# Kernel optimization log

Hardware: AMD Instinct MI355X
Metric: run time of the kernel (lower is better)

The kernel has to match this reference:

```python
import jax, jax.numpy as jnp
import numpy as np

B, T, D = 64, 2048, 512


def setup_inputs() -> dict:
    key = jax.random.key(0)
    ks = jax.random.split(key, 6)
    lim_tau = 1.0 / np.sqrt(2 * D)  # torch Linear default init bound
    lim_mem = 1.0 / np.sqrt(D)
    return {
        "x": jax.random.normal(ks[0], (B, T, D), dtype=jnp.float32),
        "tau_w": jax.random.uniform(ks[1], (D, 2 * D), jnp.float32, -lim_tau, lim_tau),
        "tau_b": jax.random.uniform(ks[2], (D,), jnp.float32, -lim_tau, lim_tau),
        "mem_w": jax.random.uniform(ks[3], (D, D), jnp.float32, -lim_mem, lim_mem),
        "mem_b": jax.random.uniform(ks[4], (D,), jnp.float32, -lim_mem, lim_mem),
        "log_thresh": jnp.zeros((D,), jnp.float32),
    }


def reference(x, tau_w, tau_b, mem_w, mem_b, log_thresh):
    b, t, d = x.shape
    thr = jax.nn.sigmoid(log_thresh)  # [D]

    def step(carry, xt):
        v, tau = carry  # each [B, D]
        # liquid time-constant gate: sigmoid(Linear([xt, tau]))
        tau = jax.nn.sigmoid(jnp.concatenate([xt, tau], axis=-1) @ tau_w.T + tau_b)
        alpha = jnp.exp(-1.0 / (tau + 1e-6))
        v = alpha * v + (1.0 - alpha) * (xt @ mem_w.T + mem_b)
        s = (v >= thr).astype(x.dtype)  # spike
        v = v * (1.0 - s)  # hard reset
        return (v, tau), s

    x_tbd = jnp.swapaxes(x, 0, 1)  # [T, B, D] for scan
    init = (jnp.zeros((b, d), x.dtype), jnp.ones((b, d), x.dtype))
    (v, tau), spikes = jax.lax.scan(step, init, x_tbd)
    return jnp.swapaxes(spikes, 0, 1), tau, v  # [B,T,D], [B,D], [B,D]
```

## Files before the change

kernel.cpp:

```cpp
#include <hip/hip_runtime.h>
#include <math.h>

#define B_ 64
#define T_ 2048
#define D_ 512
#define BT_ (B_ * T_)
#define XWORDS (B_ * D_)

typedef unsigned long long u64;

__global__ void prep_weights(const float* __restrict__ tau_w,
                             const float* __restrict__ mem_w,
                             float* __restrict__ Wcat,
                             float* __restrict__ WTh) {
    int idx = blockIdx.x * 256 + threadIdx.x;
    {
        int k = idx >> 10, j = idx & 1023;
        float v = (j < 512) ? tau_w[j * 1024 + k] : mem_w[(j - 512) * 512 + k];
        Wcat[idx] = v;
    }
    if (idx < 512 * 512) {
        int k = idx >> 9, d = idx & 511;
        WTh[idx] = tau_w[d * 1024 + 512 + k];
    }
}

__global__ __launch_bounds__(256, 2)
void gemm_xw(const float* __restrict__ X, const float* __restrict__ Wc,
             const float* __restrict__ tau_b, const float* __restrict__ mem_b,
             float* __restrict__ Aout, float* __restrict__ Mout) {
    __shared__ __align__(16) float As[16][128];
    __shared__ __align__(16) float Bs[16][128];
    const int bn = blockIdx.x;
    const int bm = blockIdx.y;
    const int tid = threadIdx.x;
    const int tm = (tid >> 4) << 3;
    const int tn = (tid & 15) << 3;
    const int m0 = bm * 128, n0 = bn * 128;

    const float4* X4 = (const float4*)X;
    const float4* Wc4 = (const float4*)Wc;

    float acc[8][8];
#pragma unroll
    for (int i = 0; i < 8; i++)
#pragma unroll
        for (int j = 0; j < 8; j++) acc[i][j] = 0.0f;

    const int ar = tid >> 1;
    const int ac2 = (tid & 1) * 2;
    const int bkr = tid >> 4;
    const int bc = (tid & 15) * 2;

    for (int kt = 0; kt < 512; kt += 16) {
        float4 av0 = X4[(m0 + ar) * 128 + (kt >> 2) + ac2];
        float4 av1 = X4[(m0 + ar) * 128 + (kt >> 2) + ac2 + 1];
        float4 bv0 = Wc4[(kt + bkr) * 256 + bn * 32 + bc];
        float4 bv1 = Wc4[(kt + bkr) * 256 + bn * 32 + bc + 1];
        __syncthreads();
        As[ac2 * 4 + 0][ar] = av0.x;
        As[ac2 * 4 + 1][ar] = av0.y;
        As[ac2 * 4 + 2][ar] = av0.z;
        As[ac2 * 4 + 3][ar] = av0.w;
        As[ac2 * 4 + 4][ar] = av1.x;
        As[ac2 * 4 + 5][ar] = av1.y;
        As[ac2 * 4 + 6][ar] = av1.z;
        As[ac2 * 4 + 7][ar] = av1.w;
        *(float4*)&Bs[bkr][bc * 4] = bv0;
        *(float4*)&Bs[bkr][bc * 4 + 4] = bv1;
        __syncthreads();
#pragma unroll
        for (int kk = 0; kk < 16; kk++) {
            float4 a0 = *(const float4*)&As[kk][tm];
            float4 a1 = *(const float4*)&As[kk][tm + 4];
            float4 b0 = *(const float4*)&Bs[kk][tn];
            float4 b1 = *(const float4*)&Bs[kk][tn + 4];
            float av[8] = {a0.x, a0.y, a0.z, a0.w, a1.x, a1.y, a1.z, a1.w};
            float bv[8] = {b0.x, b0.y, b0.z, b0.w, b1.x, b1.y, b1.z, b1.w};
#pragma unroll
            for (int i = 0; i < 8; i++)
#pragma unroll
                for (int j = 0; j < 8; j++)
                    acc[i][j] = fmaf(av[i], bv[j], acc[i][j]);
        }
    }

    const bool isA = (bn < 4);
    float* Cout = isA ? Aout : Mout;
    const float* bias = isA ? tau_b : mem_b;
    const int ncol0 = (isA ? n0 : n0 - 512) + tn;
    float bj[8];
#pragma unroll
    for (int j = 0; j < 8; j++) bj[j] = bias[ncol0 + j];
#pragma unroll
    for (int i = 0; i < 8; i++) {
        size_t off = (size_t)(m0 + tm + i) * 512 + ncol0;
        float4 o0, o1;
        o0.x = acc[i][0] + bj[0]; o0.y = acc[i][1] + bj[1];
        o0.z = acc[i][2] + bj[2]; o0.w = acc[i][3] + bj[3];
        o1.x = acc[i][4] + bj[4]; o1.y = acc[i][5] + bj[5];
        o1.z = acc[i][6] + bj[6]; o1.w = acc[i][7] + bj[7];
        *(float4*)&Cout[off] = o0;
        *(float4*)&Cout[off + 4] = o1;
    }
}

__global__ void init_sync(u64* __restrict__ xchg, int* __restrict__ ctr) {
    int idx = blockIdx.x * 256 + threadIdx.x;
    if (idx < 2 * XWORDS) xchg[idx] = (idx < XWORDS) ? 0x3F800000ull : 0ull;
    if (idx < 16) ctr[idx] = 0;
}

__global__ __launch_bounds__(512)
__attribute__((amdgpu_waves_per_eu(2, 2)))
void scan_lds(const float* __restrict__ WTh,
              const float* __restrict__ Mm,
              const float* __restrict__ log_thresh,
              float* __restrict__ AmOut,
              float* __restrict__ OutTail,
              u64* __restrict__ xchg,
              int* __restrict__ ctr) {
    __shared__ __align__(16) float4 w_lds[8192];
    __shared__ __align__(16) float tau_s[2][512];
    __shared__ __align__(16) float part[2][16][64];
    __shared__ int role_s;

    const int tid = threadIdx.x;

    if (tid == 0) {
        unsigned xcd;
        asm volatile("s_getreg_b32 %0, hwreg(HW_REG_XCC_ID)" : "=s"(xcd));
        xcd &= 7;
        int rank = atomicAdd(&ctr[xcd], 1) & 31;
        role_s = ((rank & 7) << 8) | ((int)xcd * 4 + (rank >> 3));
    }
    __syncthreads();
    const int sg = role_s >> 8;
    const int bp = role_s & 255;

    {
        const int ch = tid & 63;
        const int kr8 = tid >> 6;
        float* wl = (float*)w_lds;
        for (int i = 0; i < 64; i++) {
            int krow = i * 8 + kr8;
            float val = WTh[krow * 512 + sg * 64 + ch];
            wl[(krow >> 2) * 256 + ch * 4 + (krow & 3)] = val;
        }
    }

    const int eb = tid >> 6;
    const int ech = tid & 63;
    const int gch = sg * 64 + ech;
    float thr = 0.f, v = 0.f, tau_keep = 0.f;
    if (tid < 128) thr = 1.0f / (1.0f + expf(-log_thresh[gch]));
    size_t abase = ((size_t)(bp * 2 + eb) * T_) * D_ + gch;

    const int cp = tid & 31;
    const int ks = tid >> 5;

    const int gb = (tid >> 7) & 1;
    const int ge = tid & 127;

    __syncthreads();

    for (int c = 1; c <= T_; c++) {
        float a_in = 0.f, m_in = 0.f;
        if (tid < 128) { a_in = AmOut[abase]; m_in = Mm[abase]; }

        if (tid < 256) {
            const u64* src = xchg + (size_t)((c - 1) & 1) * XWORDS
                                  + (bp * 2 + gb) * 512 + ge * 4;
            const unsigned tgt = (unsigned)(c - 1);
            u64 v0, v1, v2, v3;
            int guard = 0;
            do {
                v0 = __hip_atomic_load(src + 0, __ATOMIC_RELAXED,
                                       __HIP_MEMORY_SCOPE_AGENT);
                v1 = __hip_atomic_load(src + 1, __ATOMIC_RELAXED,
                                       __HIP_MEMORY_SCOPE_AGENT);
                v2 = __hip_atomic_load(src + 2, __ATOMIC_RELAXED,
                                       __HIP_MEMORY_SCOPE_AGENT);
                v3 = __hip_atomic_load(src + 3, __ATOMIC_RELAXED,
                                       __HIP_MEMORY_SCOPE_AGENT);
            } while ((((unsigned)(v0 >> 32) < tgt) |
                      ((unsigned)(v1 >> 32) < tgt) |
                      ((unsigned)(v2 >> 32) < tgt) |
                      ((unsigned)(v3 >> 32) < tgt)) && ++guard < (1 << 22));
            float4 tv = make_float4(__uint_as_float((unsigned)v0),
                                    __uint_as_float((unsigned)v1),
                                    __uint_as_float((unsigned)v2),
                                    __uint_as_float((unsigned)v3));
            *(float4*)&tau_s[gb][ge * 4] = tv;
        }
        __syncthreads();

        float acc00 = 0.f, acc01 = 0.f, acc10 = 0.f, acc11 = 0.f;
#pragma unroll
        for (int q = 0; q < 8; q++) {
            const int qq = ks * 8 + q;
            float4 wA = w_lds[qq * 64 + cp];
            float4 wB = w_lds[qq * 64 + cp + 32];
            float4 t0 = *(const float4*)&tau_s[0][qq * 4];
            float4 t1 = *(const float4*)&tau_s[1][qq * 4];
            acc00 = fmaf(t0.x, wA.x, acc00); acc00 = fmaf(t0.y, wA.y, acc00);
            acc00 = fmaf(t0.z, wA.z, acc00); acc00 = fmaf(t0.w, wA.w, acc00);
            acc01 = fmaf(t0.x, wB.x, acc01); acc01 = fmaf(t0.y, wB.y, acc01);
            acc01 = fmaf(t0.z, wB.z, acc01); acc01 = fmaf(t0.w, wB.w, acc01);
            acc10 = fmaf(t1.x, wA.x, acc10); acc10 = fmaf(t1.y, wA.y, acc10);
            acc10 = fmaf(t1.z, wA.z, acc10); acc10 = fmaf(t1.w, wA.w, acc10);
            acc11 = fmaf(t1.x, wB.x, acc11); acc11 = fmaf(t1.y, wB.y, acc11);
            acc11 = fmaf(t1.z, wB.z, acc11); acc11 = fmaf(t1.w, wB.w, acc11);
        }
        part[0][ks][cp]      = acc00;
        part[0][ks][cp + 32] = acc01;
        part[1][ks][cp]      = acc10;
        part[1][ks][cp + 32] = acc11;
        __syncthreads();

        if (tid < 128) {
            float sum = 0.f;
#pragma unroll
            for (int j = 0; j < 16; j++) sum += part[eb][j][ech];
            float pre = sum + a_in;
            float tau = 1.0f / (1.0f + expf(-pre));
            float alpha = expf(-1.0f / (tau + 1e-6f));
            v = alpha * v + (1.0f - alpha) * m_in;
            float s = (v >= thr) ? 1.0f : 0.0f;
            AmOut[abase] = s;
            v = v * (1.0f - s);
            tau_keep = tau;
            u64 pack = ((u64)(unsigned)c << 32) | (u64)__float_as_uint(tau);
            __hip_atomic_store(&xchg[(size_t)(c & 1) * XWORDS
                                     + (bp * 2 + eb) * 512 + gch],
                               pack, __ATOMIC_RELAXED, __HIP_MEMORY_SCOPE_AGENT);
            abase += D_;
        }
    }

    if (tid < 128) {
        const size_t batch = bp * 2 + eb;
        OutTail[(size_t)BT_ * D_ + batch * D_ + gch] = tau_keep;
        OutTail[(size_t)BT_ * D_ + (size_t)B_ * D_ + batch * D_ + gch] = v;
    }
}

extern "C" void kernel_launch(void* const* d_in, const int* in_sizes, int n_in,
                              void* d_out, int out_size, void* d_ws, size_t ws_size,
                              hipStream_t stream) {
    (void)in_sizes; (void)n_in; (void)out_size; (void)ws_size;
    const float* x          = (const float*)d_in[0];
    const float* tau_w      = (const float*)d_in[1];
    const float* tau_b      = (const float*)d_in[2];
    const float* mem_w      = (const float*)d_in[3];
    const float* mem_b      = (const float*)d_in[4];
    const float* log_thresh = (const float*)d_in[5];
    float* out = (float*)d_out;

    float* Wcat = (float*)d_ws;
    float* WTh  = Wcat + 512 * 1024;
    float* Mout = WTh + 512 * 512;
    u64* xchg = (u64*)d_ws;
    int* ctr  = (int*)((char*)d_ws + 2 * XWORDS * sizeof(u64));

    float* Aout = out;

    prep_weights<<<2048, 256, 0, stream>>>(tau_w, mem_w, Wcat, WTh);
    gemm_xw<<<dim3(8, 1024), 256, 0, stream>>>(x, Wcat, tau_b, mem_b, Aout, Mout);
    init_sync<<<256, 256, 0, stream>>>(xchg, ctr);

    const float* WThc = WTh;
    const float* Mmc  = Mout;
    const float* ltc  = log_thresh;
    float* outp = out;
    u64* xchgp = xchg;
    int* ctrp = ctr;
    void* args[7] = {(void*)&WThc, (void*)&Mmc, (void*)&ltc,
                     (void*)&Aout, (void*)&outp, (void*)&xchgp, (void*)&ctrp};
    hipLaunchCooperativeKernel((const void*)scan_lds, dim3(256), dim3(512),
                               args, 0, stream);
}
```

Measured before the change: 6.442 ms.

## Make each wave poll its own tau slice and take own-group tau from LDS

Each of the 8 waves now polls the exchange buffer only for the 64-channel k-slice it reduces over, with a wave barrier in place of the block barrier. A wave then waits on a single producer group instead of the whole block waiting on all 512 channels. The block's own group skips polling and reads its tau directly from LDS, which is written after each step. This adds a block barrier at the end of each step but lets waves whose producers arrive early start their partial dot products sooner.

```diff
diff --git a/kernel.cpp b/kernel.cpp
--- a/kernel.cpp
+++ b/kernel.cpp
@@ -113,13 +113,13 @@
 
 __global__ __launch_bounds__(512)
 __attribute__((amdgpu_waves_per_eu(2, 2)))
-void scan_lds(const float* __restrict__ WTh,
-              const float* __restrict__ Mm,
-              const float* __restrict__ log_thresh,
-              float* __restrict__ AmOut,
-              float* __restrict__ OutTail,
-              u64* __restrict__ xchg,
-              int* __restrict__ ctr) {
+void scan_wave(const float* __restrict__ WTh,
+               const float* __restrict__ Mm,
+               const float* __restrict__ log_thresh,
+               float* __restrict__ AmOut,
+               float* __restrict__ OutTail,
+               u64* __restrict__ xchg,
+               int* __restrict__ ctr) {
     __shared__ __align__(16) float4 w_lds[8192];
     __shared__ __align__(16) float tau_s[2][512];
     __shared__ __align__(16) float part[2][16][64];
@@ -149,6 +149,12 @@
         }
     }
 
+    const int ws = tid >> 6;
+    const int lane = tid & 63;
+    const int cp = lane & 31;
+    const int kh = lane >> 5;
+    const bool self = (ws == sg);
+
     const int eb = tid >> 6;
     const int ech = tid & 63;
     const int gch = sg * 64 + ech;
@@ -156,53 +162,40 @@
     if (tid < 128) thr = 1.0f / (1.0f + expf(-log_thresh[gch]));
     size_t abase = ((size_t)(bp * 2 + eb) * T_) * D_ + gch;
 
-    const int cp = tid & 31;
-    const int ks = tid >> 5;
-
-    const int gb = (tid >> 7) & 1;
-    const int ge = tid & 127;
-
+    if (tid < 128) tau_s[eb][sg * 64 + ech] = 1.0f;
     __syncthreads();
 
     for (int c = 1; c <= T_; c++) {
         float a_in = 0.f, m_in = 0.f;
         if (tid < 128) { a_in = AmOut[abase]; m_in = Mm[abase]; }
 
-        if (tid < 256) {
-            const u64* src = xchg + (size_t)((c - 1) & 1) * XWORDS
-                                  + (bp * 2 + gb) * 512 + ge * 4;
+        if (!self) {
+            const u64* s0 = xchg + (size_t)((c - 1) & 1) * XWORDS
+                                 + (size_t)(bp * 2) * 512 + ws * 64 + lane;
+            const u64* s1 = s0 + 512;
             const unsigned tgt = (unsigned)(c - 1);
-            u64 v0, v1, v2, v3;
+            u64 v0, v1;
             int guard = 0;
             do {
-                v0 = __hip_atomic_load(src + 0, __ATOMIC_RELAXED,
+                v0 = __hip_atomic_load(s0, __ATOMIC_RELAXED,
                                        __HIP_MEMORY_SCOPE_AGENT);
-                v1 = __hip_atomic_load(src + 1, __ATOMIC_RELAXED,
-                                       __HIP_MEMORY_SCOPE_AGENT);
-                v2 = __hip_atomic_load(src + 2, __ATOMIC_RELAXED,
-                                       __HIP_MEMORY_SCOPE_AGENT);
-                v3 = __hip_atomic_load(src + 3, __ATOMIC_RELAXED,
+                v1 = __hip_atomic_load(s1, __ATOMIC_RELAXED,
                                        __HIP_MEMORY_SCOPE_AGENT);
             } while ((((unsigned)(v0 >> 32) < tgt) |
-                      ((unsigned)(v1 >> 32) < tgt) |
-                      ((unsigned)(v2 >> 32) < tgt) |
-                      ((unsigned)(v3 >> 32) < tgt)) && ++guard < (1 << 22));
-            float4 tv = make_float4(__uint_as_float((unsigned)v0),
-                                    __uint_as_float((unsigned)v1),
-                                    __uint_as_float((unsigned)v2),
-                                    __uint_as_float((unsigned)v3));
-            *(float4*)&tau_s[gb][ge * 4] = tv;
-        }
-        __syncthreads();
+                      ((unsigned)(v1 >> 32) < tgt)) && ++guard < (1 << 22));
+            tau_s[0][ws * 64 + lane] = __uint_as_float((unsigned)v0);
+            tau_s[1][ws * 64 + lane] = __uint_as_float((unsigned)v1);
+        }
+        __builtin_amdgcn_wave_barrier();
 
         float acc00 = 0.f, acc01 = 0.f, acc10 = 0.f, acc11 = 0.f;
 #pragma unroll
         for (int q = 0; q < 8; q++) {
-            const int qq = ks * 8 + q;
+            const int qq = ws * 16 + kh * 8 + q;
             float4 wA = w_lds[qq * 64 + cp];
             float4 wB = w_lds[qq * 64 + cp + 32];
-            float4 t0 = *(const float4*)&tau_s[0][qq * 4];
-            float4 t1 = *(const float4*)&tau_s[1][qq * 4];
+            float4 t0 = *(const float4*)&tau_s[0][ws * 64 + kh * 32 + q * 4];
+            float4 t1 = *(const float4*)&tau_s[1][ws * 64 + kh * 32 + q * 4];
             acc00 = fmaf(t0.x, wA.x, acc00); acc00 = fmaf(t0.y, wA.y, acc00);
             acc00 = fmaf(t0.z, wA.z, acc00); acc00 = fmaf(t0.w, wA.w, acc00);
             acc01 = fmaf(t0.x, wB.x, acc01); acc01 = fmaf(t0.y, wB.y, acc01);
@@ -212,10 +205,11 @@
             acc11 = fmaf(t1.x, wB.x, acc11); acc11 = fmaf(t1.y, wB.y, acc11);
             acc11 = fmaf(t1.z, wB.z, acc11); acc11 = fmaf(t1.w, wB.w, acc11);
         }
-        part[0][ks][cp]      = acc00;
-        part[0][ks][cp + 32] = acc01;
-        part[1][ks][cp]      = acc10;
-        part[1][ks][cp + 32] = acc11;
+        const int slot = ws * 2 + kh;
+        part[0][slot][cp]      = acc00;
+        part[0][slot][cp + 32] = acc01;
+        part[1][slot][cp]      = acc10;
+        part[1][slot][cp + 32] = acc11;
         __syncthreads();
 
         if (tid < 128) {
@@ -230,12 +224,14 @@
             AmOut[abase] = s;
             v = v * (1.0f - s);
             tau_keep = tau;
+            tau_s[eb][sg * 64 + ech] = tau;
             u64 pack = ((u64)(unsigned)c << 32) | (u64)__float_as_uint(tau);
             __hip_atomic_store(&xchg[(size_t)(c & 1) * XWORDS
                                      + (bp * 2 + eb) * 512 + gch],
                                pack, __ATOMIC_RELAXED, __HIP_MEMORY_SCOPE_AGENT);
             abase += D_;
         }
+        __syncthreads();
     }
 
     if (tid < 128) {
@@ -277,6 +273,6 @@
     int* ctrp = ctr;
     void* args[7] = {(void*)&WThc, (void*)&Mmc, (void*)&ltc,
                      (void*)&Aout, (void*)&outp, (void*)&xchgp, (void*)&ctrp};
-    hipLaunchCooperativeKernel((const void*)scan_lds, dim3(256), dim3(512),
+    hipLaunchCooperativeKernel((const void*)scan_wave, dim3(256), dim3(512),
                                args, 0, stream);
 }
```

Result: faster. 5.411 ms (-16.0%).
